# Kernel optimization log

Hardware: AMD Instinct MI355X
Metric: run time of the kernel (lower is better)

## Reference

```python
import jax, jax.numpy as jnp
import numpy as np

B, H, S, D = 2, 16, 2048, 64

def setup_inputs() -> dict:
    key = jax.random.key(0)
    kq, kk, kv = jax.random.split(key, 3)
    q = jax.random.normal(kq, (B, H, S, D), dtype=jnp.float32)
    k = jax.random.normal(kk, (B, H, S, D), dtype=jnp.float32)
    v = jax.random.normal(kv, (B, H, S, D), dtype=jnp.float32)
    # causal mask, True = attend
    mask = jnp.broadcast_to(jnp.tril(jnp.ones((S, S), dtype=bool)), (B, H, S, S))
    return {"q": q, "k": k, "v": v, "mask": mask}

def reference(q, k, v, mask):
    dim = q.shape[-1]
    scale = 1.0 / jnp.sqrt(jnp.asarray(dim, q.dtype))
    scores = jnp.einsum('bhqd,bhkd->bhqk', q, k) * scale  # [B,H,S,S]
    scores = jnp.where(mask, scores, jnp.finfo(scores.dtype).min)
    probs = jax.nn.softmax(scores, axis=-1)
    return jnp.einsum('bhqk,bhkd->bhqd', probs, v)
```

## Files before the change

### kernel.cpp

```cpp
#include <hip/hip_runtime.h>

#define B_   2
#define H_   16
#define S_   2048
#define D_   64
#define BQ   128
#define BK   64
#define NW   8
#define QSCALE 0.18033688011112042f
#define DEFER_THR 8.0f

typedef _Float16 f16x4 __attribute__((ext_vector_type(4)));
typedef _Float16 f16x8 __attribute__((ext_vector_type(8)));
typedef float    f32x4 __attribute__((ext_vector_type(4)));

typedef const unsigned int __attribute__((address_space(1))) gu32;
typedef unsigned int       __attribute__((address_space(3))) lu32;

#define KBYTES_PER_HEAD (S_ * 128)
#define WS_V_OFF ((size_t)B_ * H_ * KBYTES_PER_HEAD)
#define WS_NEED  (2 * WS_V_OFF)

__global__ __launch_bounds__(256) void prep_kv(const float* __restrict__ K,
                                               const float* __restrict__ V,
                                               char* __restrict__ ws)
{
    if (blockIdx.x < (B_ * H_ * S_ * 8) / 256) {
        const int gidx = blockIdx.x * 256 + threadIdx.x;
        const int gcol = gidx & 7;
        const int srow = gidx >> 3;
        const float4* src = (const float4*)(K + (size_t)srow * D_ + gcol * 8);
        float4 a = src[0], b = src[1];
        f16x8 h;
        h[0] = (_Float16)a.x; h[1] = (_Float16)a.y; h[2] = (_Float16)a.z; h[3] = (_Float16)a.w;
        h[4] = (_Float16)b.x; h[5] = (_Float16)b.y; h[6] = (_Float16)b.z; h[7] = (_Float16)b.w;
        const int s  = srow & (S_ - 1);
        const int bh = srow >> 11;
        size_t off = (size_t)bh * KBYTES_PER_HEAD + (size_t)(s >> 6) * 8192
                   + (s & 63) * 128 + ((gcol ^ (s & 7)) << 4);
        *(f16x8*)(ws + off) = h;
    } else {
        __shared__ _Float16 Vl[64][72];
        const int tile = blockIdx.x - (B_ * H_ * S_ * 8) / 256;
        const int bh = tile >> 5, t = tile & 31;
        const float* vb = V + ((size_t)bh * S_ + t * 64) * D_;
        const int tid = threadIdx.x;
        #pragma unroll
        for (int it = 0; it < 2; ++it) {
            const int row = (tid >> 3) + it * 32;
            const int c8  = (tid & 7) * 8;
            const float4* p = (const float4*)(vb + row * D_ + c8);
            float4 a = p[0], b = p[1];
            f16x8 h;
            h[0] = (_Float16)a.x; h[1] = (_Float16)a.y; h[2] = (_Float16)a.z; h[3] = (_Float16)a.w;
            h[4] = (_Float16)b.x; h[5] = (_Float16)b.y; h[6] = (_Float16)b.z; h[7] = (_Float16)b.w;
            *(f16x8*)&Vl[row][c8] = h;
        }
        __syncthreads();
        char* out = ws + WS_V_OFF + (size_t)bh * KBYTES_PER_HEAD + t * 8192;
        #pragma unroll
        for (int it = 0; it < 2; ++it) {
            const int task = tid + it * 256;
            const int d = task >> 3, kg = task & 7;
            f16x8 h;
            #pragma unroll
            for (int j = 0; j < 8; ++j) h[j] = Vl[kg * 8 + j][d];
            *(f16x8*)(out + d * 128 + ((kg ^ (d & 7)) << 4)) = h;
        }
    }
}


template<bool MASK>
__device__ __forceinline__ void qk_tile(
    const _Float16* __restrict__ Kb, const f16x8 aq[2], f32x4 (&accS)[4],
    int g, int l15, int sx, int dq)
{
    #pragma unroll
    for (int s = 0; s < 4; ++s) accS[s] = (f32x4){0.f, 0.f, 0.f, 0.f};
    __builtin_amdgcn_s_setprio(1);
    #pragma unroll
    for (int sub = 0; sub < 4; ++sub) {
        if (MASK && (sub * 16 > dq + 15)) continue;
        #pragma unroll
        for (int kc = 0; kc < 2; ++kc) {
            f16x8 ak = *(const f16x8*)(Kb + ((sub * 16 + l15) * 64 + (((kc * 4 + g) ^ sx) << 3)));
            accS[sub] = __builtin_amdgcn_mfma_f32_16x16x32_f16(ak, aq[kc], accS[sub], 0, 0, 0);
        }
    }
    __builtin_amdgcn_s_setprio(0);
}

template<bool MASK>
__device__ __forceinline__ void smpv_tile(
    const _Float16* __restrict__ SMb, _Float16 (*__restrict__ Plw)[72],
    f32x4 (&accS)[4], f32x4 accO[4], float& m_r, float& l_r,
    int g, int l15, int sx, int dq)
{
    const _Float16* Vb = SMb + 4096;

    auto msk = [&](int sub, int r) -> float {
        float s = accS[sub][r];
        if (MASK) {
            if (sub * 16 > dq + 15) s = -1e30f;
            else if (sub * 16 + 15 > dq) {
                if (sub * 16 + g * 4 + r > dq + l15) s = -1e30f;
            }
        }
        return s;
    };

    float pmax = -1e30f;
    #pragma unroll
    for (int sub = 0; sub < 4; ++sub)
        #pragma unroll
        for (int r = 0; r < 4; ++r) pmax = fmaxf(pmax, msk(sub, r));

    if (!__all(pmax <= m_r + DEFER_THR)) {
        float mx = pmax;
        mx = fmaxf(mx, __shfl_xor(mx, 16));
        mx = fmaxf(mx, __shfl_xor(mx, 32));
        const float mnew  = fmaxf(m_r, mx);
        const float alpha = __builtin_amdgcn_exp2f(m_r - mnew);
        l_r *= alpha;
        #pragma unroll
        for (int d = 0; d < 4; ++d)
            #pragma unroll
            for (int r = 0; r < 4; ++r) accO[d][r] *= alpha;
        m_r = mnew;
    }

    float rs = 0.f;
    #pragma unroll
    for (int sub = 0; sub < 4; ++sub) {
        float p0 = __builtin_amdgcn_exp2f(msk(sub, 0) - m_r);
        float p1 = __builtin_amdgcn_exp2f(msk(sub, 1) - m_r);
        float p2 = __builtin_amdgcn_exp2f(msk(sub, 2) - m_r);
        float p3 = __builtin_amdgcn_exp2f(msk(sub, 3) - m_r);
        rs += (p0 + p1) + (p2 + p3);
        f16x4 q4;
        q4[0] = (_Float16)p0; q4[1] = (_Float16)p1;
        q4[2] = (_Float16)p2; q4[3] = (_Float16)p3;
        *(f16x4*)&Plw[l15][sub * 16 + g * 4] = q4;
    }
    l_r += rs;

    asm volatile("s_waitcnt lgkmcnt(0)" ::: "memory");
    __builtin_amdgcn_sched_barrier(0);

    f16x8 pb0 = *(const f16x8*)&Plw[l15][g * 8];
    f16x8 pb1 = *(const f16x8*)&Plw[l15][32 + g * 8];

    __builtin_amdgcn_s_setprio(1);
    #pragma unroll
    for (int d = 0; d < 4; ++d) {
        f16x8 av0 = *(const f16x8*)(Vb + ((d * 16 + l15) * 64 + (((0 * 4 + g) ^ sx) << 3)));
        accO[d] = __builtin_amdgcn_mfma_f32_16x16x32_f16(av0, pb0, accO[d], 0, 0, 0);
        f16x8 av1 = *(const f16x8*)(Vb + ((d * 16 + l15) * 64 + (((1 * 4 + g) ^ sx) << 3)));
        accO[d] = __builtin_amdgcn_mfma_f32_16x16x32_f16(av1, pb1, accO[d], 0, 0, 0);
    }
    __builtin_amdgcn_s_setprio(0);
}

__global__ __launch_bounds__(512, 4) void attn_main(
    const float* __restrict__ Q, const char* __restrict__ ws, float* __restrict__ O)
{
    __shared__ _Float16 SM[3][8192];
    __shared__ _Float16 Pl[NW][16][72];

    const int tid  = threadIdx.x;
    const int lane = tid & 63;
    const int w    = tid >> 6;
    const int g    = lane >> 4;
    const int l15  = lane & 15;
    const int sx   = l15 & 7;

    const int id    = blockIdx.x;
    const int bh    = id & 31;
    const int qi    = id >> 5;
    const int qt    = (id < 256) ? (15 - qi) : (qi - 8);
    const int qbase = qt * BQ;

    const char* kbase = ws + (size_t)bh * KBYTES_PER_HEAD;
    const char* vbase = ws + WS_V_OFF + (size_t)bh * KBYTES_PER_HEAD;

    f16x8 aq[2];
    {
        const float* qrow = Q + ((size_t)bh * S_ + qbase + w * 16 + l15) * D_;
        #pragma unroll
        for (int kc = 0; kc < 2; ++kc) {
            const float4* p = (const float4*)(qrow + kc * 32 + g * 8);
            float4 x0 = p[0], x1 = p[1];
            f16x8 h;
            h[0] = (_Float16)(x0.x * QSCALE); h[1] = (_Float16)(x0.y * QSCALE);
            h[2] = (_Float16)(x0.z * QSCALE); h[3] = (_Float16)(x0.w * QSCALE);
            h[4] = (_Float16)(x1.x * QSCALE); h[5] = (_Float16)(x1.y * QSCALE);
            h[6] = (_Float16)(x1.z * QSCALE); h[7] = (_Float16)(x1.w * QSCALE);
            aq[kc] = h;
        }
    }

    f32x4 accO[4];
    #pragma unroll
    for (int i = 0; i < 4; ++i) accO[i] = (f32x4){0.f, 0.f, 0.f, 0.f};
    float m_r = -1e30f, l_r = 0.f;
    f32x4 accSA[4], accSB[4];

    const int nt  = 2 * qt + 2;
    const int dqw = qbase + w * 16;

    _Float16* bQK = &SM[0][0];
    _Float16* bST = &SM[1][0];
    _Float16* bPV = &SM[2][0];

    auto STAGE = [&](int t, _Float16* dst) {
        #pragma unroll
        for (int i = 0; i < 2; ++i) {
            const int c = w * 2 + i;
            const char* src = (c < 8 ? kbase + (size_t)t * 8192 + c * 1024
                                     : vbase + (size_t)t * 8192 + (c - 8) * 1024) + lane * 16;
            __builtin_amdgcn_global_load_lds((gu32*)src, (lu32*)(dst + c * 512), 16, 0, 0);
        }
    };
    auto SYNC = []() {
        asm volatile("s_waitcnt vmcnt(0)" ::: "memory");
        __builtin_amdgcn_s_barrier();
    };
    auto ROT = [&]() { _Float16* tmp = bPV; bPV = bQK; bQK = bST; bST = tmp; };

    STAGE(0, bQK);

    SYNC();
    STAGE(1, bST);
    if (qt == 0) qk_tile<true >(bQK, aq, accSA, g, l15, sx, dqw);
    else         qk_tile<false>(bQK, aq, accSA, g, l15, sx, 0);
    ROT();

    SYNC();
    if (nt > 2) STAGE(2, bST);
    if (qt == 0) {
        qk_tile<true >(bQK, aq, accSB, g, l15, sx, dqw - 64);
        smpv_tile<true >(bPV, Pl[w], accSA, accO, m_r, l_r, g, l15, sx, dqw);
    } else {
        qk_tile<false>(bQK, aq, accSB, g, l15, sx, 0);
        smpv_tile<false>(bPV, Pl[w], accSA, accO, m_r, l_r, g, l15, sx, 0);
    }
    ROT();

    for (int i = 1; i < qt; ++i) {
        const int t0 = 2 * i;
        SYNC();
        STAGE(t0 + 1, bST);
        qk_tile<false>(bQK, aq, accSA, g, l15, sx, 0);
        smpv_tile<false>(bPV, Pl[w], accSB, accO, m_r, l_r, g, l15, sx, 0);
        ROT();
        SYNC();
        STAGE(t0 + 2, bST);
        qk_tile<false>(bQK, aq, accSB, g, l15, sx, 0);
        smpv_tile<false>(bPV, Pl[w], accSA, accO, m_r, l_r, g, l15, sx, 0);
        ROT();
    }

    if (qt >= 1) {
        SYNC();
        STAGE(nt - 1, bST);
        qk_tile<true >(bQK, aq, accSA, g, l15, sx, dqw - (nt - 2) * 64);
        smpv_tile<false>(bPV, Pl[w], accSB, accO, m_r, l_r, g, l15, sx, 0);
        ROT();
        SYNC();
        qk_tile<true >(bQK, aq, accSB, g, l15, sx, dqw - (nt - 1) * 64);
        smpv_tile<true >(bPV, Pl[w], accSA, accO, m_r, l_r, g, l15, sx, dqw - (nt - 2) * 64);
        ROT();
    }

    smpv_tile<true>(bPV, Pl[w], accSB, accO, m_r, l_r, g, l15, sx, dqw - (nt - 1) * 64);

    float l = l_r;
    l += __shfl_xor(l, 16);
    l += __shfl_xor(l, 32);
    const float inv = 1.0f / l;
    float* orow = O + ((size_t)bh * S_ + qbase + w * 16 + l15) * D_;
    #pragma unroll
    for (int d = 0; d < 4; ++d) {
        f32x4 o = accO[d] * inv;
        *(f32x4*)&orow[d * 16 + g * 4] = o;
    }
}

extern "C" void kernel_launch(void* const* d_in, const int* in_sizes, int n_in,
                              void* d_out, int out_size, void* d_ws, size_t ws_size,
                              hipStream_t stream) {
    const float* q = (const float*)d_in[0];
    const float* k = (const float*)d_in[1];
    const float* v = (const float*)d_in[2];
    float* o = (float*)d_out;
    char* ws = (char*)d_ws;

    if (ws_size < WS_NEED) return;

    const int kblocks = (B_ * H_ * S_ * 8) / 256;
    const int vblocks = B_ * H_ * (S_ / 64);
    prep_kv<<<kblocks + vblocks, 256, 0, stream>>>(k, v, ws);
    attn_main<<<(S_ / BQ) * B_ * H_, 512, 0, stream>>>(q, ws, o);
}
```

Baseline: 50.93 us.

## Halve query tile and split each KV tile's keys across two warp groups

Reduces the query block from 128 to 64 rows, which doubles the grid size. The eight warps now form four query strips times two key halves: each warp processes 32 of the 64 keys in every staged K/V tile and keeps its own online-softmax state. At the end the two halves are merged through shared memory using max-rescaling. This aims to improve load balance and occupancy under the causal mask, at the cost of staging K/V twice as often per query row and adding a final cross-warp reduction.

```diff
diff --git a/kernel.cpp b/kernel.cpp
--- a/kernel.cpp
+++ b/kernel.cpp
@@ -4,8 +4,7 @@
 #define H_   16
 #define S_   2048
 #define D_   64
-#define BQ   128
-#define BK   64
+#define BQ   64
 #define NW   8
 #define QSCALE 0.18033688011112042f
 #define DEFER_THR 8.0f
@@ -73,18 +72,19 @@
 
 template<bool MASK>
 __device__ __forceinline__ void qk_tile(
-    const _Float16* __restrict__ Kb, const f16x8 aq[2], f32x4 (&accS)[4],
-    int g, int l15, int sx, int dq)
+    const _Float16* __restrict__ Kb, const f16x8 aq[2], f32x4 (&accS)[2],
+    int g, int l15, int sx, int kh, int dqt)
 {
     #pragma unroll
-    for (int s = 0; s < 4; ++s) accS[s] = (f32x4){0.f, 0.f, 0.f, 0.f};
+    for (int s = 0; s < 2; ++s) accS[s] = (f32x4){0.f, 0.f, 0.f, 0.f};
     __builtin_amdgcn_s_setprio(1);
     #pragma unroll
-    for (int sub = 0; sub < 4; ++sub) {
-        if (MASK && (sub * 16 > dq + 15)) continue;
+    for (int sub = 0; sub < 2; ++sub) {
+        if (MASK && (sub * 16 > dqt + 15)) continue;
         #pragma unroll
         for (int kc = 0; kc < 2; ++kc) {
-            f16x8 ak = *(const f16x8*)(Kb + ((sub * 16 + l15) * 64 + (((kc * 4 + g) ^ sx) << 3)));
+            f16x8 ak = *(const f16x8*)(Kb + ((kh * 32 + sub * 16 + l15) * 64
+                                             + (((kc * 4 + g) ^ sx) << 3)));
             accS[sub] = __builtin_amdgcn_mfma_f32_16x16x32_f16(ak, aq[kc], accS[sub], 0, 0, 0);
         }
     }
@@ -93,26 +93,23 @@
 
 template<bool MASK>
 __device__ __forceinline__ void smpv_tile(
-    const _Float16* __restrict__ SMb, _Float16 (*__restrict__ Plw)[72],
-    f32x4 (&accS)[4], f32x4 accO[4], float& m_r, float& l_r,
-    int g, int l15, int sx, int dq)
+    const _Float16* __restrict__ SMb, _Float16 (*__restrict__ Plw)[40],
+    f32x4 (&accS)[2], f32x4 accO[4], float& m_r, float& l_r,
+    int g, int l15, int sx, int kh, int dqt)
 {
     const _Float16* Vb = SMb + 4096;
 
     auto msk = [&](int sub, int r) -> float {
         float s = accS[sub][r];
         if (MASK) {
-            if (sub * 16 > dq + 15) s = -1e30f;
-            else if (sub * 16 + 15 > dq) {
-                if (sub * 16 + g * 4 + r > dq + l15) s = -1e30f;
-            }
+            if (sub * 16 + g * 4 + r > dqt + l15) s = -1e30f;
         }
         return s;
     };
 
     float pmax = -1e30f;
     #pragma unroll
-    for (int sub = 0; sub < 4; ++sub)
+    for (int sub = 0; sub < 2; ++sub)
         #pragma unroll
         for (int r = 0; r < 4; ++r) pmax = fmaxf(pmax, msk(sub, r));
 
@@ -132,7 +129,7 @@
 
     float rs = 0.f;
     #pragma unroll
-    for (int sub = 0; sub < 4; ++sub) {
+    for (int sub = 0; sub < 2; ++sub) {
         float p0 = __builtin_amdgcn_exp2f(msk(sub, 0) - m_r);
         float p1 = __builtin_amdgcn_exp2f(msk(sub, 1) - m_r);
         float p2 = __builtin_amdgcn_exp2f(msk(sub, 2) - m_r);
@@ -148,16 +145,13 @@
     asm volatile("s_waitcnt lgkmcnt(0)" ::: "memory");
     __builtin_amdgcn_sched_barrier(0);
 
-    f16x8 pb0 = *(const f16x8*)&Plw[l15][g * 8];
-    f16x8 pb1 = *(const f16x8*)&Plw[l15][32 + g * 8];
+    f16x8 pb = *(const f16x8*)&Plw[l15][g * 8];
 
     __builtin_amdgcn_s_setprio(1);
     #pragma unroll
     for (int d = 0; d < 4; ++d) {
-        f16x8 av0 = *(const f16x8*)(Vb + ((d * 16 + l15) * 64 + (((0 * 4 + g) ^ sx) << 3)));
-        accO[d] = __builtin_amdgcn_mfma_f32_16x16x32_f16(av0, pb0, accO[d], 0, 0, 0);
-        f16x8 av1 = *(const f16x8*)(Vb + ((d * 16 + l15) * 64 + (((1 * 4 + g) ^ sx) << 3)));
-        accO[d] = __builtin_amdgcn_mfma_f32_16x16x32_f16(av1, pb1, accO[d], 0, 0, 0);
+        f16x8 av = *(const f16x8*)(Vb + ((d * 16 + l15) * 64 + (((kh * 4 + g) ^ sx) << 3)));
+        accO[d] = __builtin_amdgcn_mfma_f32_16x16x32_f16(av, pb, accO[d], 0, 0, 0);
     }
     __builtin_amdgcn_s_setprio(0);
 }
@@ -166,11 +160,13 @@
     const float* __restrict__ Q, const char* __restrict__ ws, float* __restrict__ O)
 {
     __shared__ _Float16 SM[3][8192];
-    __shared__ _Float16 Pl[NW][16][72];
+    __shared__ _Float16 Pl[NW][16][40];
 
     const int tid  = threadIdx.x;
     const int lane = tid & 63;
     const int w    = tid >> 6;
+    const int st   = w & 3;
+    const int kh   = w >> 2;
     const int g    = lane >> 4;
     const int l15  = lane & 15;
     const int sx   = l15 & 7;
@@ -178,7 +174,7 @@
     const int id    = blockIdx.x;
     const int bh    = id & 31;
     const int qi    = id >> 5;
-    const int qt    = (id < 256) ? (15 - qi) : (qi - 8);
+    const int qt    = (id < 512) ? (31 - qi) : (qi - 16);
     const int qbase = qt * BQ;
 
     const char* kbase = ws + (size_t)bh * KBYTES_PER_HEAD;
@@ -186,7 +182,7 @@
 
     f16x8 aq[2];
     {
-        const float* qrow = Q + ((size_t)bh * S_ + qbase + w * 16 + l15) * D_;
+        const float* qrow = Q + ((size_t)bh * S_ + qbase + st * 16 + l15) * D_;
         #pragma unroll
         for (int kc = 0; kc < 2; ++kc) {
             const float4* p = (const float4*)(qrow + kc * 32 + g * 8);
@@ -204,10 +200,10 @@
     #pragma unroll
     for (int i = 0; i < 4; ++i) accO[i] = (f32x4){0.f, 0.f, 0.f, 0.f};
     float m_r = -1e30f, l_r = 0.f;
-    f32x4 accSA[4], accSB[4];
-
-    const int nt  = 2 * qt + 2;
-    const int dqw = qbase + w * 16;
+    f32x4 accSA[2], accSB[2];
+
+    const int nt   = qt + 1;
+    const int dqtD = st * 16 - kh * 32 + qbase - (nt - 1) * 64;
 
     _Float16* bQK = &SM[0][0];
     _Float16* bST = &SM[1][0];
@@ -231,59 +227,79 @@
     STAGE(0, bQK);
 
     SYNC();
-    STAGE(1, bST);
-    if (qt == 0) qk_tile<true >(bQK, aq, accSA, g, l15, sx, dqw);
-    else         qk_tile<false>(bQK, aq, accSA, g, l15, sx, 0);
+    if (nt > 1) STAGE(1, bST);
+    if (nt == 1) qk_tile<true >(bQK, aq, accSA, g, l15, sx, kh, dqtD);
+    else         qk_tile<false>(bQK, aq, accSA, g, l15, sx, kh, 0);
     ROT();
 
-    SYNC();
-    if (nt > 2) STAGE(2, bST);
-    if (qt == 0) {
-        qk_tile<true >(bQK, aq, accSB, g, l15, sx, dqw - 64);
-        smpv_tile<true >(bPV, Pl[w], accSA, accO, m_r, l_r, g, l15, sx, dqw);
+    int t = 1;
+    for (; t + 2 < nt; t += 2) {
+        SYNC();
+        STAGE(t + 1, bST);
+        qk_tile<false>(bQK, aq, accSB, g, l15, sx, kh, 0);
+        smpv_tile<false>(bPV, Pl[w], accSA, accO, m_r, l_r, g, l15, sx, kh, 0);
+        ROT();
+        SYNC();
+        STAGE(t + 2, bST);
+        qk_tile<false>(bQK, aq, accSA, g, l15, sx, kh, 0);
+        smpv_tile<false>(bPV, Pl[w], accSB, accO, m_r, l_r, g, l15, sx, kh, 0);
+        ROT();
+    }
+
+    if (t == nt - 2) {
+        SYNC();
+        STAGE(t + 1, bST);
+        qk_tile<false>(bQK, aq, accSB, g, l15, sx, kh, 0);
+        smpv_tile<false>(bPV, Pl[w], accSA, accO, m_r, l_r, g, l15, sx, kh, 0);
+        ROT();
+        SYNC();
+        qk_tile<true >(bQK, aq, accSA, g, l15, sx, kh, dqtD);
+        smpv_tile<false>(bPV, Pl[w], accSB, accO, m_r, l_r, g, l15, sx, kh, 0);
+        ROT();
+        smpv_tile<true>(bPV, Pl[w], accSA, accO, m_r, l_r, g, l15, sx, kh, dqtD);
+    } else if (t == nt - 1) {
+        SYNC();
+        qk_tile<true >(bQK, aq, accSB, g, l15, sx, kh, dqtD);
+        smpv_tile<false>(bPV, Pl[w], accSA, accO, m_r, l_r, g, l15, sx, kh, 0);
+        ROT();
+        smpv_tile<true>(bPV, Pl[w], accSB, accO, m_r, l_r, g, l15, sx, kh, dqtD);
     } else {
-        qk_tile<false>(bQK, aq, accSB, g, l15, sx, 0);
-        smpv_tile<false>(bPV, Pl[w], accSA, accO, m_r, l_r, g, l15, sx, 0);
-    }
-    ROT();
-
-    for (int i = 1; i < qt; ++i) {
-        const int t0 = 2 * i;
-        SYNC();
-        STAGE(t0 + 1, bST);
-        qk_tile<false>(bQK, aq, accSA, g, l15, sx, 0);
-        smpv_tile<false>(bPV, Pl[w], accSB, accO, m_r, l_r, g, l15, sx, 0);
-        ROT();
-        SYNC();
-        STAGE(t0 + 2, bST);
-        qk_tile<false>(bQK, aq, accSB, g, l15, sx, 0);
-        smpv_tile<false>(bPV, Pl[w], accSA, accO, m_r, l_r, g, l15, sx, 0);
-        ROT();
-    }
-
-    if (qt >= 1) {
-        SYNC();
-        STAGE(nt - 1, bST);
-        qk_tile<true >(bQK, aq, accSA, g, l15, sx, dqw - (nt - 2) * 64);
-        smpv_tile<false>(bPV, Pl[w], accSB, accO, m_r, l_r, g, l15, sx, 0);
-        ROT();
-        SYNC();
-        qk_tile<true >(bQK, aq, accSB, g, l15, sx, dqw - (nt - 1) * 64);
-        smpv_tile<true >(bPV, Pl[w], accSA, accO, m_r, l_r, g, l15, sx, dqw - (nt - 2) * 64);
-        ROT();
-    }
-
-    smpv_tile<true>(bPV, Pl[w], accSB, accO, m_r, l_r, g, l15, sx, dqw - (nt - 1) * 64);
-
-    float l = l_r;
-    l += __shfl_xor(l, 16);
-    l += __shfl_xor(l, 32);
-    const float inv = 1.0f / l;
-    float* orow = O + ((size_t)bh * S_ + qbase + w * 16 + l15) * D_;
-    #pragma unroll
-    for (int d = 0; d < 4; ++d) {
-        f32x4 o = accO[d] * inv;
-        *(f32x4*)&orow[d * 16 + g * 4] = o;
+        smpv_tile<true>(bPV, Pl[w], accSA, accO, m_r, l_r, g, l15, sx, kh, dqtD);
+    }
+
+    float* M = (float*)&SM[0][0];
+    __syncthreads();
+    if (kh == 1) {
+        float* base = M + st * 1152;
+        #pragma unroll
+        for (int d = 0; d < 4; ++d)
+            #pragma unroll
+            for (int r = 0; r < 4; ++r)
+                base[(d * 4 + r) * 64 + lane] = accO[d][r];
+        base[1024 + lane] = l_r;
+        base[1088 + lane] = m_r;
+    }
+    __syncthreads();
+    if (kh == 0) {
+        float* base = M + st * 1152;
+        const float m_b = base[1088 + lane];
+        const float l_b = base[1024 + lane];
+        const float m   = fmaxf(m_r, m_b);
+        const float sA  = __builtin_amdgcn_exp2f(m_r - m);
+        const float sB  = __builtin_amdgcn_exp2f(m_b - m);
+        float l = l_r * sA + l_b * sB;
+        l += __shfl_xor(l, 16);
+        l += __shfl_xor(l, 32);
+        const float inv = 1.0f / l;
+        float* orow = O + ((size_t)bh * S_ + qbase + st * 16 + l15) * D_;
+        #pragma unroll
+        for (int d = 0; d < 4; ++d) {
+            f32x4 o;
+            #pragma unroll
+            for (int r = 0; r < 4; ++r)
+                o[r] = (accO[d][r] * sA + base[(d * 4 + r) * 64 + lane] * sB) * inv;
+            *(f32x4*)&orow[d * 16 + g * 4] = o;
+        }
     }
 }
 
```

Result: slower. 54.91 us (+7.8%).

## Load V fragments directly from global into registers instead of LDS staging

Applied to the files above, without the earlier changes.

V tiles are no longer staged through shared memory. Each wave now reads its V MFMA operands straight from the pre-converted global workspace into registers, and the prep kernel drops the XOR swizzle on the V layout. This halves the LDS ring buffer, which may help occupancy and cut LDS traffic and staging work. The cost is per-wave global loads (many waves read the same V data, relying on cache), extra VGPR pressure for eight f16x8 fragments, and global latency exposed close to the PV MFMAs.

```diff
diff --git a/kernel.cpp b/kernel.cpp
--- a/kernel.cpp
+++ b/kernel.cpp
@@ -5,7 +5,6 @@
 #define S_   2048
 #define D_   64
 #define BQ   128
-#define BK   64
 #define NW   8
 #define QSCALE 0.18033688011112042f
 #define DEFER_THR 8.0f
@@ -65,7 +64,7 @@
             f16x8 h;
             #pragma unroll
             for (int j = 0; j < 8; ++j) h[j] = Vl[kg * 8 + j][d];
-            *(f16x8*)(out + d * 128 + ((kg ^ (d & 7)) << 4)) = h;
+            *(f16x8*)(out + d * 128 + kg * 16) = h;
         }
     }
 }
@@ -93,12 +92,10 @@
 
 template<bool MASK>
 __device__ __forceinline__ void smpv_tile(
-    const _Float16* __restrict__ SMb, _Float16 (*__restrict__ Plw)[72],
+    const f16x8 av0[4], const f16x8 av1[4], _Float16 (*__restrict__ Plw)[72],
     f32x4 (&accS)[4], f32x4 accO[4], float& m_r, float& l_r,
-    int g, int l15, int sx, int dq)
+    int g, int l15, int dq)
 {
-    const _Float16* Vb = SMb + 4096;
-
     auto msk = [&](int sub, int r) -> float {
         float s = accS[sub][r];
         if (MASK) {
@@ -153,19 +150,18 @@
 
     __builtin_amdgcn_s_setprio(1);
     #pragma unroll
-    for (int d = 0; d < 4; ++d) {
-        f16x8 av0 = *(const f16x8*)(Vb + ((d * 16 + l15) * 64 + (((0 * 4 + g) ^ sx) << 3)));
-        accO[d] = __builtin_amdgcn_mfma_f32_16x16x32_f16(av0, pb0, accO[d], 0, 0, 0);
-        f16x8 av1 = *(const f16x8*)(Vb + ((d * 16 + l15) * 64 + (((1 * 4 + g) ^ sx) << 3)));
-        accO[d] = __builtin_amdgcn_mfma_f32_16x16x32_f16(av1, pb1, accO[d], 0, 0, 0);
-    }
+    for (int d = 0; d < 4; ++d)
+        accO[d] = __builtin_amdgcn_mfma_f32_16x16x32_f16(av0[d], pb0, accO[d], 0, 0, 0);
+    #pragma unroll
+    for (int d = 0; d < 4; ++d)
+        accO[d] = __builtin_amdgcn_mfma_f32_16x16x32_f16(av1[d], pb1, accO[d], 0, 0, 0);
     __builtin_amdgcn_s_setprio(0);
 }
 
 __global__ __launch_bounds__(512, 4) void attn_main(
     const float* __restrict__ Q, const char* __restrict__ ws, float* __restrict__ O)
 {
-    __shared__ _Float16 SM[3][8192];
+    __shared__ _Float16 SM[3][4096];
     __shared__ _Float16 Pl[NW][16][72];
 
     const int tid  = threadIdx.x;
@@ -205,28 +201,30 @@
     for (int i = 0; i < 4; ++i) accO[i] = (f32x4){0.f, 0.f, 0.f, 0.f};
     float m_r = -1e30f, l_r = 0.f;
     f32x4 accSA[4], accSB[4];
+    f16x8 av0[4], av1[4];
 
     const int nt  = 2 * qt + 2;
     const int dqw = qbase + w * 16;
 
     _Float16* bQK = &SM[0][0];
     _Float16* bST = &SM[1][0];
-    _Float16* bPV = &SM[2][0];
+    _Float16* bSP = &SM[2][0];
 
     auto STAGE = [&](int t, _Float16* dst) {
-        #pragma unroll
-        for (int i = 0; i < 2; ++i) {
-            const int c = w * 2 + i;
-            const char* src = (c < 8 ? kbase + (size_t)t * 8192 + c * 1024
-                                     : vbase + (size_t)t * 8192 + (c - 8) * 1024) + lane * 16;
-            __builtin_amdgcn_global_load_lds((gu32*)src, (lu32*)(dst + c * 512), 16, 0, 0);
-        }
+        const char* src = kbase + (size_t)t * 8192 + w * 1024 + lane * 16;
+        __builtin_amdgcn_global_load_lds((gu32*)src, (lu32*)(dst + w * 512), 16, 0, 0);
+    };
+    auto LOADV = [&](int t, f16x8 (&av)[4], int kc) {
+        const char* vt = vbase + (size_t)t * 8192 + ((kc * 4 + g) << 4) + l15 * 128;
+        #pragma unroll
+        for (int d = 0; d < 4; ++d)
+            av[d] = *(const f16x8*)(vt + d * 2048);
     };
     auto SYNC = []() {
         asm volatile("s_waitcnt vmcnt(0)" ::: "memory");
         __builtin_amdgcn_s_barrier();
     };
-    auto ROT = [&]() { _Float16* tmp = bPV; bPV = bQK; bQK = bST; bST = tmp; };
+    auto ROT = [&]() { _Float16* tmp = bSP; bSP = bQK; bQK = bST; bST = tmp; };
 
     STAGE(0, bQK);
 
@@ -237,43 +235,56 @@
     ROT();
 
     SYNC();
+    LOADV(0, av0, 0);
     if (nt > 2) STAGE(2, bST);
     if (qt == 0) {
         qk_tile<true >(bQK, aq, accSB, g, l15, sx, dqw - 64);
-        smpv_tile<true >(bPV, Pl[w], accSA, accO, m_r, l_r, g, l15, sx, dqw);
+        LOADV(0, av1, 1);
+        smpv_tile<true >(av0, av1, Pl[w], accSA, accO, m_r, l_r, g, l15, dqw);
     } else {
         qk_tile<false>(bQK, aq, accSB, g, l15, sx, 0);
-        smpv_tile<false>(bPV, Pl[w], accSA, accO, m_r, l_r, g, l15, sx, 0);
+        LOADV(0, av1, 1);
+        smpv_tile<false>(av0, av1, Pl[w], accSA, accO, m_r, l_r, g, l15, 0);
     }
     ROT();
 
     for (int i = 1; i < qt; ++i) {
         const int t0 = 2 * i;
         SYNC();
+        LOADV(t0 - 1, av0, 0);
         STAGE(t0 + 1, bST);
         qk_tile<false>(bQK, aq, accSA, g, l15, sx, 0);
-        smpv_tile<false>(bPV, Pl[w], accSB, accO, m_r, l_r, g, l15, sx, 0);
+        LOADV(t0 - 1, av1, 1);
+        smpv_tile<false>(av0, av1, Pl[w], accSB, accO, m_r, l_r, g, l15, 0);
         ROT();
         SYNC();
+        LOADV(t0, av0, 0);
         STAGE(t0 + 2, bST);
         qk_tile<false>(bQK, aq, accSB, g, l15, sx, 0);
-        smpv_tile<false>(bPV, Pl[w], accSA, accO, m_r, l_r, g, l15, sx, 0);
+        LOADV(t0, av1, 1);
+        smpv_tile<false>(av0, av1, Pl[w], accSA, accO, m_r, l_r, g, l15, 0);
         ROT();
     }
 
     if (qt >= 1) {
         SYNC();
+        LOADV(nt - 3, av0, 0);
         STAGE(nt - 1, bST);
         qk_tile<true >(bQK, aq, accSA, g, l15, sx, dqw - (nt - 2) * 64);
-        smpv_tile<false>(bPV, Pl[w], accSB, accO, m_r, l_r, g, l15, sx, 0);
+        LOADV(nt - 3, av1, 1);
+        smpv_tile<false>(av0, av1, Pl[w], accSB, accO, m_r, l_r, g, l15, 0);
         ROT();
         SYNC();
+        LOADV(nt - 2, av0, 0);
         qk_tile<true >(bQK, aq, accSB, g, l15, sx, dqw - (nt - 1) * 64);
-        smpv_tile<true >(bPV, Pl[w], accSA, accO, m_r, l_r, g, l15, sx, dqw - (nt - 2) * 64);
+        LOADV(nt - 2, av1, 1);
+        smpv_tile<true >(av0, av1, Pl[w], accSA, accO, m_r, l_r, g, l15, dqw - (nt - 2) * 64);
         ROT();
     }
 
-    smpv_tile<true>(bPV, Pl[w], accSB, accO, m_r, l_r, g, l15, sx, dqw - (nt - 1) * 64);
+    LOADV(nt - 1, av0, 0);
+    LOADV(nt - 1, av1, 1);
+    smpv_tile<true>(av0, av1, Pl[w], accSB, accO, m_r, l_r, g, l15, dqw - (nt - 1) * 64);
 
     float l = l_r;
     l += __shfl_xor(l, 16);
```

After: 90.47 us. 1.78x slower.

## Permute key-row mapping so QK output feeds PV MFMA directly from registers

Applied to the files above, without the earlier changes.

Reorders which K rows each lane loads in the QK MFMA so that the score accumulator layout matches the B-operand layout of the PV MFMA. Probabilities are packed straight into registers instead of being written to and read back from a per-wave LDS scratch buffer, removing the LDS round trip, the lgkmcnt wait and the scheduling barrier. Mask index computation is updated to the permuted key order. This also frees the Pl shared-memory array, which may help occupancy, at the cost of a less regular K-row access pattern with a different swizzle.

```diff
diff --git a/kernel.cpp b/kernel.cpp
--- a/kernel.cpp
+++ b/kernel.cpp
@@ -5,12 +5,10 @@
 #define S_   2048
 #define D_   64
 #define BQ   128
-#define BK   64
 #define NW   8
 #define QSCALE 0.18033688011112042f
 #define DEFER_THR 8.0f
 
-typedef _Float16 f16x4 __attribute__((ext_vector_type(4)));
 typedef _Float16 f16x8 __attribute__((ext_vector_type(8)));
 typedef float    f32x4 __attribute__((ext_vector_type(4)));
 
@@ -70,21 +68,23 @@
     }
 }
 
-
 template<bool MASK>
 __device__ __forceinline__ void qk_tile(
     const _Float16* __restrict__ Kb, const f16x8 aq[2], f32x4 (&accS)[4],
-    int g, int l15, int sx, int dq)
+    int g, int l15, int dq)
 {
+    const int rbase = 8 * (l15 >> 2) + (l15 & 3);
     #pragma unroll
     for (int s = 0; s < 4; ++s) accS[s] = (f32x4){0.f, 0.f, 0.f, 0.f};
     __builtin_amdgcn_s_setprio(1);
     #pragma unroll
     for (int sub = 0; sub < 4; ++sub) {
-        if (MASK && (sub * 16 > dq + 15)) continue;
+        if (MASK && (32 * (sub >> 1) + 4 * (sub & 1) > dq + 15)) continue;
+        const int kr  = rbase + 4 * (sub & 1) + 32 * (sub >> 1);
+        const int sxk = (l15 & 3) + 4 * (sub & 1);
         #pragma unroll
         for (int kc = 0; kc < 2; ++kc) {
-            f16x8 ak = *(const f16x8*)(Kb + ((sub * 16 + l15) * 64 + (((kc * 4 + g) ^ sx) << 3)));
+            f16x8 ak = *(const f16x8*)(Kb + (kr * 64 + (((kc * 4 + g) ^ sxk) << 3)));
             accS[sub] = __builtin_amdgcn_mfma_f32_16x16x32_f16(ak, aq[kc], accS[sub], 0, 0, 0);
         }
     }
@@ -93,7 +93,7 @@
 
 template<bool MASK>
 __device__ __forceinline__ void smpv_tile(
-    const _Float16* __restrict__ SMb, _Float16 (*__restrict__ Plw)[72],
+    const _Float16* __restrict__ SMb,
     f32x4 (&accS)[4], f32x4 accO[4], float& m_r, float& l_r,
     int g, int l15, int sx, int dq)
 {
@@ -102,10 +102,8 @@
     auto msk = [&](int sub, int r) -> float {
         float s = accS[sub][r];
         if (MASK) {
-            if (sub * 16 > dq + 15) s = -1e30f;
-            else if (sub * 16 + 15 > dq) {
-                if (sub * 16 + g * 4 + r > dq + l15) s = -1e30f;
-            }
+            const int kk = 32 * (sub >> 1) + 8 * g + 4 * (sub & 1) + r;
+            if (kk > dq + l15) s = -1e30f;
         }
         return s;
     };
@@ -131,6 +129,7 @@
     }
 
     float rs = 0.f;
+    f16x8 pb0, pb1;
     #pragma unroll
     for (int sub = 0; sub < 4; ++sub) {
         float p0 = __builtin_amdgcn_exp2f(msk(sub, 0) - m_r);
@@ -138,18 +137,21 @@
         float p2 = __builtin_amdgcn_exp2f(msk(sub, 2) - m_r);
         float p3 = __builtin_amdgcn_exp2f(msk(sub, 3) - m_r);
         rs += (p0 + p1) + (p2 + p3);
-        f16x4 q4;
-        q4[0] = (_Float16)p0; q4[1] = (_Float16)p1;
-        q4[2] = (_Float16)p2; q4[3] = (_Float16)p3;
-        *(f16x4*)&Plw[l15][sub * 16 + g * 4] = q4;
+        if (sub == 0) {
+            pb0[0] = (_Float16)p0; pb0[1] = (_Float16)p1;
+            pb0[2] = (_Float16)p2; pb0[3] = (_Float16)p3;
+        } else if (sub == 1) {
+            pb0[4] = (_Float16)p0; pb0[5] = (_Float16)p1;
+            pb0[6] = (_Float16)p2; pb0[7] = (_Float16)p3;
+        } else if (sub == 2) {
+            pb1[0] = (_Float16)p0; pb1[1] = (_Float16)p1;
+            pb1[2] = (_Float16)p2; pb1[3] = (_Float16)p3;
+        } else {
+            pb1[4] = (_Float16)p0; pb1[5] = (_Float16)p1;
+            pb1[6] = (_Float16)p2; pb1[7] = (_Float16)p3;
+        }
     }
     l_r += rs;
-
-    asm volatile("s_waitcnt lgkmcnt(0)" ::: "memory");
-    __builtin_amdgcn_sched_barrier(0);
-
-    f16x8 pb0 = *(const f16x8*)&Plw[l15][g * 8];
-    f16x8 pb1 = *(const f16x8*)&Plw[l15][32 + g * 8];
 
     __builtin_amdgcn_s_setprio(1);
     #pragma unroll
@@ -166,7 +168,6 @@
     const float* __restrict__ Q, const char* __restrict__ ws, float* __restrict__ O)
 {
     __shared__ _Float16 SM[3][8192];
-    __shared__ _Float16 Pl[NW][16][72];
 
     const int tid  = threadIdx.x;
     const int lane = tid & 63;
@@ -232,18 +233,18 @@
 
     SYNC();
     STAGE(1, bST);
-    if (qt == 0) qk_tile<true >(bQK, aq, accSA, g, l15, sx, dqw);
-    else         qk_tile<false>(bQK, aq, accSA, g, l15, sx, 0);
+    if (qt == 0) qk_tile<true >(bQK, aq, accSA, g, l15, dqw);
+    else         qk_tile<false>(bQK, aq, accSA, g, l15, 0);
     ROT();
 
     SYNC();
     if (nt > 2) STAGE(2, bST);
     if (qt == 0) {
-        qk_tile<true >(bQK, aq, accSB, g, l15, sx, dqw - 64);
-        smpv_tile<true >(bPV, Pl[w], accSA, accO, m_r, l_r, g, l15, sx, dqw);
+        qk_tile<true >(bQK, aq, accSB, g, l15, dqw - 64);
+        smpv_tile<true >(bPV, accSA, accO, m_r, l_r, g, l15, sx, dqw);
     } else {
-        qk_tile<false>(bQK, aq, accSB, g, l15, sx, 0);
-        smpv_tile<false>(bPV, Pl[w], accSA, accO, m_r, l_r, g, l15, sx, 0);
+        qk_tile<false>(bQK, aq, accSB, g, l15, 0);
+        smpv_tile<false>(bPV, accSA, accO, m_r, l_r, g, l15, sx, 0);
     }
     ROT();
 
@@ -251,29 +252,29 @@
         const int t0 = 2 * i;
         SYNC();
         STAGE(t0 + 1, bST);
-        qk_tile<false>(bQK, aq, accSA, g, l15, sx, 0);
-        smpv_tile<false>(bPV, Pl[w], accSB, accO, m_r, l_r, g, l15, sx, 0);
+        qk_tile<false>(bQK, aq, accSA, g, l15, 0);
+        smpv_tile<false>(bPV, accSB, accO, m_r, l_r, g, l15, sx, 0);
         ROT();
         SYNC();
         STAGE(t0 + 2, bST);
-        qk_tile<false>(bQK, aq, accSB, g, l15, sx, 0);
-        smpv_tile<false>(bPV, Pl[w], accSA, accO, m_r, l_r, g, l15, sx, 0);
+        qk_tile<false>(bQK, aq, accSB, g, l15, 0);
+        smpv_tile<false>(bPV, accSA, accO, m_r, l_r, g, l15, sx, 0);
         ROT();
     }
 
     if (qt >= 1) {
         SYNC();
         STAGE(nt - 1, bST);
-        qk_tile<true >(bQK, aq, accSA, g, l15, sx, dqw - (nt - 2) * 64);
-        smpv_tile<false>(bPV, Pl[w], accSB, accO, m_r, l_r, g, l15, sx, 0);
+        qk_tile<true >(bQK, aq, accSA, g, l15, dqw - (nt - 2) * 64);
+        smpv_tile<false>(bPV, accSB, accO, m_r, l_r, g, l15, sx, 0);
         ROT();
         SYNC();
-        qk_tile<true >(bQK, aq, accSB, g, l15, sx, dqw - (nt - 1) * 64);
-        smpv_tile<true >(bPV, Pl[w], accSA, accO, m_r, l_r, g, l15, sx, dqw - (nt - 2) * 64);
+        qk_tile<true >(bQK, aq, accSB, g, l15, dqw - (nt - 1) * 64);
+        smpv_tile<true >(bPV, accSA, accO, m_r, l_r, g, l15, sx, dqw - (nt - 2) * 64);
         ROT();
     }
 
-    smpv_tile<true>(bPV, Pl[w], accSB, accO, m_r, l_r, g, l15, sx, dqw - (nt - 1) * 64);
+    smpv_tile<true>(bPV, accSB, accO, m_r, l_r, g, l15, sx, dqw - (nt - 1) * 64);
 
     float l = l_r;
     l += __shfl_xor(l, 16);
```

After: 48.01 us. -5.7%, faster.
